# Optimization experiments

Hardware: AMD Instinct MI355X
Metric: run time of the kernel (lower is better)

Reference implementation:

```python
import jax, jax.numpy as jnp
import numpy as np

D = 384      # embedding_dim
H = 6        # num_heads
HD = D // H  # head_dim = 64
S = 256      # seq_len
B = 64       # batch
EPS = 1e-5


def setup_inputs() -> dict:
    key = jax.random.key(0)
    ks = jax.random.split(key, 16)
    scale = 0.02
    inp = {
        'x': jax.random.normal(ks[0], (B, S, D), dtype=jnp.float32),
        'wq': jax.random.normal(ks[1], (D, D), dtype=jnp.float32) * scale,
        'wk': jax.random.normal(ks[2], (D, D), dtype=jnp.float32) * scale,
        'wv': jax.random.normal(ks[3], (D, D), dtype=jnp.float32) * scale,
        'wo': jax.random.normal(ks[4], (D, D), dtype=jnp.float32) * scale,
        'bo': jnp.zeros((D,), dtype=jnp.float32),
        'w1': jax.random.normal(ks[5], (D, 4 * D), dtype=jnp.float32) * scale,
        'b1': jnp.zeros((4 * D,), dtype=jnp.float32),
        'w2': jax.random.normal(ks[6], (4 * D, D), dtype=jnp.float32) * scale,
        'b2': jnp.zeros((D,), dtype=jnp.float32),
        'g1': jnp.ones((D,), dtype=jnp.float32),
        'be1': jnp.zeros((D,), dtype=jnp.float32),
        'g2': jnp.ones((D,), dtype=jnp.float32),
        'be2': jnp.zeros((D,), dtype=jnp.float32),
    }
    return inp


def _layernorm(x, g, b):
    m = jnp.mean(x, axis=-1, keepdims=True)
    v = jnp.mean((x - m) ** 2, axis=-1, keepdims=True)
    return (x - m) * jax.lax.rsqrt(v + EPS) * g + b


def _block(x, wq, wk, wv, wo, bo, w1, b1, w2, b2, g1, be1, g2, be2):
    b, s, d = x.shape
    h = _layernorm(x, g1, be1)
    # batched per-head projections (equivalent to 6 separate small Linears concatenated)
    q = (h @ wq).reshape(b, s, H, HD).transpose(0, 2, 1, 3)  # [B,H,S,HD]
    k = (h @ wk).reshape(b, s, H, HD).transpose(0, 2, 1, 3)
    v = (h @ wv).reshape(b, s, H, HD).transpose(0, 2, 1, 3)
    scores = jnp.einsum('bhqe,bhke->bhqk', q, k) / np.float32(np.sqrt(HD))
    causal = jnp.tril(jnp.ones((s, s), dtype=bool))
    scores = jnp.where(causal, scores, -jnp.inf)
    attn = jax.nn.softmax(scores, axis=-1)  # dropout = identity in eval
    ctx = jnp.einsum('bhqk,bhke->bhqe', attn, v)  # [B,H,S,HD]
    ctx = ctx.transpose(0, 2, 1, 3).reshape(b, s, d)  # concat heads
    x = x + (ctx @ wo + bo)
    h2 = _layernorm(x, g2, be2)
    ff = jax.nn.relu(h2 @ w1 + b1) @ w2 + b2
    return x + ff


def reference(x, wq, wk, wv, wo, bo, w1, b1, w2, b2, g1, be1, g2, be2):
    return _block(x, wq, wk, wv, wo, bo, w1, b1, w2, b2, g1, be1, g2, be2)
```

## Files before the change

kernel.cpp:

```cpp
#include <hip/hip_runtime.h>
#include <hip/hip_bf16.h>

typedef __hip_bfloat16 bf16;
typedef __attribute__((ext_vector_type(8))) short short8;
typedef __attribute__((ext_vector_type(4))) float f32x4;

#define D_EMB 384
#define NHEAD 6
#define HDIM 64
#define SEQ 256
#define BATCH 64
#define M_ROWS (BATCH * SEQ)
#define DFF (4 * D_EMB)
#define DQKV (3 * D_EMB)

__device__ __forceinline__ void async_load16(const void* gptr, void* lptr) {
    __builtin_amdgcn_global_load_lds(
        (const __attribute__((address_space(1))) unsigned int*)gptr,
        (__attribute__((address_space(3))) unsigned int*)lptr, 16, 0, 0);
}

__global__ __launch_bounds__(256)
void transpose_all(const float* __restrict__ wq, const float* __restrict__ wk,
                   const float* __restrict__ wv, const float* __restrict__ wo,
                   const float* __restrict__ w1, const float* __restrict__ w2,
                   bf16* __restrict__ wqkv_t, bf16* __restrict__ wo_t,
                   bf16* __restrict__ w1_t, bf16* __restrict__ w2_t)
{
    __shared__ float t[32][33];
    const int id = blockIdx.x;
    const float* src; bf16* dst; int K, N, local, nbT;
    if      (id <  144) { src = wq; dst = wqkv_t;               K = 384;  N = 384;  local = id;        nbT = 12; }
    else if (id <  288) { src = wk; dst = wqkv_t + 147456;      K = 384;  N = 384;  local = id - 144;  nbT = 12; }
    else if (id <  432) { src = wv; dst = wqkv_t + 294912;      K = 384;  N = 384;  local = id - 288;  nbT = 12; }
    else if (id <  576) { src = wo; dst = wo_t;                 K = 384;  N = 384;  local = id - 432;  nbT = 12; }
    else if (id < 1152) { src = w1; dst = w1_t;                 K = 384;  N = 1536; local = id - 576;  nbT = 48; }
    else                { src = w2; dst = w2_t;                 K = 1536; N = 384;  local = id - 1152; nbT = 12; }
    const int nb = (local % nbT) * 32, kb = (local / nbT) * 32;
    const int tx = threadIdx.x, ty = threadIdx.y;
#pragma unroll
    for (int i = 0; i < 32; i += 8)
        t[ty + i][tx] = src[(size_t)(kb + ty + i) * N + nb + tx];
    __syncthreads();
#pragma unroll
    for (int i = 0; i < 32; i += 8)
        dst[(size_t)(nb + ty + i) * K + kb + tx] = __float2bfloat16(t[tx][ty + i]);
}

__global__ __launch_bounds__(256)
void ln_kernel(const float* __restrict__ x, const float* __restrict__ g,
               const float* __restrict__ be, bf16* __restrict__ out)
{
    const int row  = blockIdx.x * 4 + (threadIdx.x >> 6);
    const int lane = threadIdx.x & 63;
    const float* xr = x + (size_t)row * D_EMB;

    float v[6];
    float s = 0.f;
#pragma unroll
    for (int i = 0; i < 6; ++i) { v[i] = xr[lane + i * 64]; s += v[i]; }
#pragma unroll
    for (int off = 32; off; off >>= 1) s += __shfl_xor(s, off, 64);
    const float mean = s * (1.f / 384.f);

    float var = 0.f;
#pragma unroll
    for (int i = 0; i < 6; ++i) { float d = v[i] - mean; var += d * d; }
#pragma unroll
    for (int off = 32; off; off >>= 1) var += __shfl_xor(var, off, 64);
    const float rstd = rsqrtf(var * (1.f / 384.f) + 1e-5f);

    bf16* orow = out + (size_t)row * D_EMB;
#pragma unroll
    for (int i = 0; i < 6; ++i) {
        const int c = lane + i * 64;
        orow[c] = __float2bfloat16((v[i] - mean) * rstd * g[c] + be[c]);
    }
}

template<bool RELU, bool OUT_BF16, bool VT>
__global__ __launch_bounds__(256)
void mfma_gemm(const bf16* __restrict__ A, const bf16* __restrict__ Bt,
               const float* __restrict__ bias, const float* __restrict__ res,
               void* __restrict__ Cout, int M, int N, int K, bf16* __restrict__ vt)
{
    __shared__ __attribute__((aligned(16))) unsigned short smem[32768];
    unsigned short* As = smem;
    unsigned short* Bs = smem + 16384;

    const int tid  = threadIdx.x;
    const int wave = tid >> 6;
    const int lane = tid & 63;

    const int nwg = gridDim.x * gridDim.y;
    const int bl  = blockIdx.y * gridDim.x + blockIdx.x;
    const int lb  = (bl & 7) * (nwg >> 3) + (bl >> 3);
    const int m0  = (lb / gridDim.x) * 128;
    const int n0  = (lb % gridDim.x) * 128;

    const int wm = (wave >> 1) * 64;
    const int wn = (wave & 1) * 64;
    const int c16 = lane & 15;
    const int g   = lane >> 4;
    const int lr  = lane >> 3;
    const int ls  = lane & 7;

    f32x4 acc[4][4];
#pragma unroll
    for (int i = 0; i < 4; ++i)
#pragma unroll
        for (int j = 0; j < 4; ++j)
            acc[i][j] = (f32x4){0.f, 0.f, 0.f, 0.f};

    auto stage = [&](int buf, int k0) {
#pragma unroll
        for (int it = 0; it < 4; ++it) {
            const int r = (it * 4 + wave) * 8 + lr;
            const int oct = ls ^ (r & 7);
            async_load16(A + (size_t)(m0 + r) * K + k0 + oct * 8,
                         &As[buf * 8192 + (it * 4 + wave) * 512]);
            async_load16(Bt + (size_t)(n0 + r) * K + k0 + oct * 8,
                         &Bs[buf * 8192 + (it * 4 + wave) * 512]);
        }
    };

    stage(0, 0);
    const int KT = K >> 6;
    for (int kt = 0; kt < KT; ++kt) {
        const int cur = kt & 1;
        __syncthreads();
        if (kt + 1 < KT) stage(cur ^ 1, (kt + 1) * 64);
#pragma unroll
        for (int kk = 0; kk < 2; ++kk) {
            short8 af[4], bfr[4];
#pragma unroll
            for (int i = 0; i < 4; ++i) {
                const int row = wm + i * 16 + c16;
                af[i] = *(const short8*)&As[cur * 8192 + row * 64 + (((kk * 4 + g) ^ (row & 7)) << 3)];
            }
#pragma unroll
            for (int j = 0; j < 4; ++j) {
                const int row = wn + j * 16 + c16;
                bfr[j] = *(const short8*)&Bs[cur * 8192 + row * 64 + (((kk * 4 + g) ^ (row & 7)) << 3)];
            }
#pragma unroll
            for (int i = 0; i < 4; ++i)
#pragma unroll
                for (int j = 0; j < 4; ++j)
                    acc[i][j] = __builtin_amdgcn_mfma_f32_16x16x32_bf16(
                        af[i], bfr[j], acc[i][j], 0, 0, 0);
        }
    }

    const int crow = g * 4;

    if (VT && n0 >= 768) {
        __syncthreads();
        unsigned short* T = smem;
#pragma unroll
        for (int j = 0; j < 4; ++j) {
            const int col = wn + j * 16 + c16;
#pragma unroll
            for (int i = 0; i < 4; ++i)
#pragma unroll
                for (int r = 0; r < 4; ++r) {
                    const int row = wm + i * 16 + crow + r;
                    bf16 pb = __float2bfloat16(acc[i][j][r]);
                    T[col * 128 + ((((row >> 3) ^ (col & 15)) << 3) | (row & 7))] =
                        *(unsigned short*)&pb;
                }
        }
        __syncthreads();
        const int b  = m0 >> 8;
        const int s0 = m0 & 255;
#pragma unroll
        for (int it = 0; it < 8; ++it) {
            const int cc = it * 256 + tid;
            const int col = cc >> 4, o = cc & 15;
            const int gcol = n0 - 768 + col;
            const int h = gcol >> 6, d = gcol & 63;
            const int so = (o ^ (col & 15)) << 3;
            const uint4 v = *(const uint4*)&T[col * 128 + o * 8];
            *(uint4*)(vt + (((size_t)(b * NHEAD + h) * 64 + d) * 256 + s0 + so)) = v;
        }
        return;
    }

    if (OUT_BF16) {
        __syncthreads();
        unsigned short* Cs = smem;
#pragma unroll
        for (int j = 0; j < 4; ++j) {
            const int col = wn + j * 16 + c16;
            const float bv = bias ? bias[n0 + col] : 0.f;
#pragma unroll
            for (int i = 0; i < 4; ++i)
#pragma unroll
                for (int r = 0; r < 4; ++r) {
                    const int row = wm + i * 16 + crow + r;
                    float v = acc[i][j][r] + bv;
                    if (RELU) v = fmaxf(v, 0.f);
                    bf16 pb = __float2bfloat16(v);
                    Cs[row * 128 + ((((col >> 3) ^ (row & 15)) << 3) | (col & 7))] =
                        *(unsigned short*)&pb;
                }
        }
        __syncthreads();
#pragma unroll
        for (int it = 0; it < 8; ++it) {
            const int cc = it * 256 + tid;
            const int row = cc >> 4, o = cc & 15;
            const uint4 v = *(const uint4*)&Cs[row * 128 + ((o ^ (row & 15)) << 3)];
            *(uint4*)((bf16*)Cout + (size_t)(m0 + row) * N + n0 + o * 8) = v;
        }
        return;
    }

#pragma unroll
    for (int j = 0; j < 4; ++j) {
        const int colg = n0 + wn + j * 16 + c16;
        const float bv = bias ? bias[colg] : 0.f;
#pragma unroll
        for (int i = 0; i < 4; ++i) {
            const int rowg = m0 + wm + i * 16 + crow;
#pragma unroll
            for (int r = 0; r < 4; ++r) {
                float v = acc[i][j][r] + bv;
                if (res) v += res[(size_t)(rowg + r) * N + colg];
                if (RELU) v = fmaxf(v, 0.f);
                ((float*)Cout)[(size_t)(rowg + r) * N + colg] = v;
            }
        }
    }
}

__global__ __launch_bounds__(256)
void mfma_gemm64(const bf16* __restrict__ A, const bf16* __restrict__ Bt,
                 const float* __restrict__ bias, const float* __restrict__ res,
                 float* __restrict__ Cout, int M, int N, int K)
{
    __shared__ __attribute__((aligned(16))) unsigned short smem[24576];
    unsigned short* As = smem;
    unsigned short* Bs = smem + 8192;

    const int tid  = threadIdx.x;
    const int wave = tid >> 6;
    const int lane = tid & 63;

    const int nwg = gridDim.x * gridDim.y;
    const int bl  = blockIdx.y * gridDim.x + blockIdx.x;
    const int lb  = (bl & 7) * (nwg >> 3) + (bl >> 3);
    const int m0  = (lb / gridDim.x) * 64;
    const int n0  = (lb % gridDim.x) * 128;

    const int wm = (wave >> 1) * 32;
    const int wn = (wave & 1) * 64;
    const int c16 = lane & 15;
    const int g   = lane >> 4;
    const int lr  = lane >> 3;
    const int ls  = lane & 7;

    f32x4 acc[2][4];
#pragma unroll
    for (int i = 0; i < 2; ++i)
#pragma unroll
        for (int j = 0; j < 4; ++j)
            acc[i][j] = (f32x4){0.f, 0.f, 0.f, 0.f};

    auto stage = [&](int buf, int k0) {
#pragma unroll
        for (int it = 0; it < 2; ++it) {
            const int r = (it * 4 + wave) * 8 + lr;
            const int oct = ls ^ (r & 7);
            async_load16(A + (size_t)(m0 + r) * K + k0 + oct * 8,
                         &As[buf * 4096 + (it * 4 + wave) * 512]);
        }
#pragma unroll
        for (int it = 0; it < 4; ++it) {
            const int r = (it * 4 + wave) * 8 + lr;
            const int oct = ls ^ (r & 7);
            async_load16(Bt + (size_t)(n0 + r) * K + k0 + oct * 8,
                         &Bs[buf * 8192 + (it * 4 + wave) * 512]);
        }
    };

    stage(0, 0);
    const int KT = K >> 6;
    for (int kt = 0; kt < KT; ++kt) {
        const int cur = kt & 1;
        __syncthreads();
        if (kt + 1 < KT) stage(cur ^ 1, (kt + 1) * 64);
#pragma unroll
        for (int kk = 0; kk < 2; ++kk) {
            short8 af[2], bfr[4];
#pragma unroll
            for (int i = 0; i < 2; ++i) {
                const int row = wm + i * 16 + c16;
                af[i] = *(const short8*)&As[cur * 4096 + row * 64 + (((kk * 4 + g) ^ (row & 7)) << 3)];
            }
#pragma unroll
            for (int j = 0; j < 4; ++j) {
                const int row = wn + j * 16 + c16;
                bfr[j] = *(const short8*)&Bs[cur * 8192 + row * 64 + (((kk * 4 + g) ^ (row & 7)) << 3)];
            }
#pragma unroll
            for (int i = 0; i < 2; ++i)
#pragma unroll
                for (int j = 0; j < 4; ++j)
                    acc[i][j] = __builtin_amdgcn_mfma_f32_16x16x32_bf16(
                        af[i], bfr[j], acc[i][j], 0, 0, 0);
        }
    }

    const int crow = g * 4;
#pragma unroll
    for (int j = 0; j < 4; ++j) {
        const int colg = n0 + wn + j * 16 + c16;
        const float bv = bias ? bias[colg] : 0.f;
#pragma unroll
        for (int i = 0; i < 2; ++i) {
            const int rowg = m0 + wm + i * 16 + crow;
#pragma unroll
            for (int r = 0; r < 4; ++r) {
                float v = acc[i][j][r] + bv;
                if (res) v += res[(size_t)(rowg + r) * N + colg];
                Cout[(size_t)(rowg + r) * N + colg] = v;
            }
        }
    }
}

#define ATT_SCALE 0.18033688f

__global__ __launch_bounds__(64, 2)
void attn_mfma(const bf16* __restrict__ qkv, const bf16* __restrict__ vt,
               bf16* __restrict__ ctx)
{
    __shared__ __attribute__((aligned(16))) unsigned short bufKP[4096];
    __shared__ __attribute__((aligned(16))) unsigned short bufV[4096];

    const int nb   = gridDim.x;
    const int bid0 = blockIdx.x;
    const int bid  = (bid0 & 7) * (nb >> 3) + (bid0 >> 3);
    const int bh = bid >> 2, qi = bid & 3;
    const int b = bh / NHEAD, h = bh % NHEAD;
    const int lane = threadIdx.x;
    const int g = lane >> 4;
    const int c = lane & 15;
    const int lr = lane >> 3;
    const int ls = lane & 7;

    const size_t qbase  = (size_t)b * SEQ * DQKV + (size_t)h * HDIM;
    const size_t vtbase = (size_t)bh * HDIM * SEQ;

    short8 qf[4][2];
#pragma unroll
    for (int i = 0; i < 4; ++i)
#pragma unroll
        for (int kf = 0; kf < 2; ++kf)
            qf[i][kf] = *(const short8*)(qkv + qbase +
                (size_t)(qi * 64 + i * 16 + c) * DQKV + kf * 32 + g * 8);

    short8 ones;
#pragma unroll
    for (int e = 0; e < 8; ++e) ones[e] = (short)0x3F80;

    f32x4 acc_o[4][4], acc_l[4];
#pragma unroll
    for (int i = 0; i < 4; ++i) {
        acc_l[i] = (f32x4){0.f, 0.f, 0.f, 0.f};
#pragma unroll
        for (int n = 0; n < 4; ++n)
            acc_o[i][n] = (f32x4){0.f, 0.f, 0.f, 0.f};
    }

    for (int jt = 0; jt <= qi; ++jt) {
#pragma unroll
        for (int it = 0; it < 8; ++it) {
            const int row = it * 8 + lr;
            const int oct = ls ^ (row & 7);
            async_load16(qkv + qbase + (size_t)(jt * 64 + row) * DQKV + D_EMB + oct * 8,
                         bufKP + it * 512);
            async_load16(vt + vtbase + (size_t)row * SEQ + jt * 64 + oct * 8,
                         bufV + it * 512);
        }
        asm volatile("s_waitcnt vmcnt(0)" ::: "memory");

        short8 kb[2][4];
#pragma unroll
        for (int kf = 0; kf < 2; ++kf)
#pragma unroll
            for (int j = 0; j < 4; ++j) {
                const int row = j * 16 + c;
                kb[kf][j] = *(const short8*)&bufKP[row * 64 + (((kf * 4 + g) ^ (row & 7)) << 3)];
            }

        const bool diag = (jt == qi);
#pragma unroll
        for (int i = 0; i < 4; ++i) {
            f32x4 s[4];
#pragma unroll
            for (int j = 0; j < 4; ++j) s[j] = (f32x4){0.f, 0.f, 0.f, 0.f};
#pragma unroll
            for (int kf = 0; kf < 2; ++kf)
#pragma unroll
                for (int j = 0; j < 4; ++j)
                    s[j] = __builtin_amdgcn_mfma_f32_16x16x32_bf16(
                        qf[i][kf], kb[kf][j], s[j], 0, 0, 0);

#pragma unroll
            for (int r = 0; r < 4; ++r) {
                const int row = i * 16 + g * 4 + r;
#pragma unroll
                for (int j = 0; j < 4; ++j) {
                    const int col = j * 16 + c;
                    float p = exp2f(s[j][r] * ATT_SCALE);
                    if (diag && col > row) p = 0.f;
                    bf16 pb = __float2bfloat16(p);
                    bufKP[row * 64 + (((col >> 3) ^ (row & 7)) << 3) + (col & 7)] =
                        *(unsigned short*)&pb;
                }
            }
        }

#pragma unroll
        for (int kf = 0; kf < 2; ++kf) {
            short8 pa[4], vb[4];
#pragma unroll
            for (int i = 0; i < 4; ++i) {
                const int row = i * 16 + c;
                pa[i] = *(const short8*)&bufKP[row * 64 + (((kf * 4 + g) ^ (row & 7)) << 3)];
            }
#pragma unroll
            for (int n = 0; n < 4; ++n) {
                const int row = n * 16 + c;
                vb[n] = *(const short8*)&bufV[row * 64 + (((kf * 4 + g) ^ (row & 7)) << 3)];
            }
#pragma unroll
            for (int i = 0; i < 4; ++i) {
#pragma unroll
                for (int n = 0; n < 4; ++n)
                    acc_o[i][n] = __builtin_amdgcn_mfma_f32_16x16x32_bf16(
                        pa[i], vb[n], acc_o[i][n], 0, 0, 0);
                acc_l[i] = __builtin_amdgcn_mfma_f32_16x16x32_bf16(
                    pa[i], ones, acc_l[i], 0, 0, 0);
            }
        }
    }

    const size_t obase = (size_t)b * SEQ * D_EMB + (size_t)h * HDIM;
#pragma unroll
    for (int i = 0; i < 4; ++i)
#pragma unroll
        for (int r = 0; r < 4; ++r) {
            const float rl = 1.f / acc_l[i][r];
            const int row = qi * 64 + i * 16 + g * 4 + r;
#pragma unroll
            for (int n = 0; n < 4; ++n) {
                const int col = n * 16 + c;
                ctx[obase + (size_t)row * D_EMB + col] =
                    __float2bfloat16(acc_o[i][n][r] * rl);
            }
        }
}

extern "C" void kernel_launch(void* const* d_in, const int* in_sizes, int n_in,
                              void* d_out, int out_size, void* d_ws, size_t ws_size,
                              hipStream_t stream)
{
    const float* x  = (const float*)d_in[0];
    const float* wq = (const float*)d_in[1];
    const float* wk = (const float*)d_in[2];
    const float* wv = (const float*)d_in[3];
    const float* wo = (const float*)d_in[4];
    const float* bo = (const float*)d_in[5];
    const float* w1 = (const float*)d_in[6];
    const float* b1 = (const float*)d_in[7];
    const float* w2 = (const float*)d_in[8];
    const float* b2 = (const float*)d_in[9];
    const float* g1  = (const float*)d_in[10];
    const float* be1 = (const float*)d_in[11];
    const float* g2  = (const float*)d_in[12];
    const float* be2 = (const float*)d_in[13];
    float* out = (float*)d_out;
    (void)in_sizes; (void)n_in; (void)out_size; (void)ws_size;

    char* w = (char*)d_ws;
    bf16* wqkv_t = (bf16*)(w);
    bf16* wo_t   = (bf16*)(w + (size_t)(1024 * 1024));
    bf16* w1_t   = (bf16*)(w + (size_t)(1536 * 1024));
    bf16* w2_t   = (bf16*)(w + (size_t)(2816 * 1024));
    char* slotA  = w + 4 * 1024 * 1024;
    char* slotB  = slotA + (size_t)M_ROWS * D_EMB * sizeof(bf16);

    bf16* h1  = (bf16*)slotA;
    bf16* ctx = (bf16*)slotA;
    bf16* h2  = (bf16*)slotA;
    bf16* qkv = (bf16*)slotB;
    bf16* vt  = (bf16*)slotB + (size_t)M_ROWS * DQKV;
    bf16* ff1 = (bf16*)slotB;

    const dim3 blk(256);

    transpose_all<<<dim3(1728), dim3(32, 8), 0, stream>>>(
        wq, wk, wv, wo, w1, w2, wqkv_t, wo_t, w1_t, w2_t);

    ln_kernel<<<dim3(M_ROWS / 4), blk, 0, stream>>>(x, g1, be1, h1);

    mfma_gemm<false, true, true><<<dim3(DQKV / 128, M_ROWS / 128), blk, 0, stream>>>(
        h1, wqkv_t, nullptr, nullptr, qkv, M_ROWS, DQKV, D_EMB, vt);

    attn_mfma<<<dim3(BATCH * NHEAD * 4), dim3(64), 0, stream>>>(qkv, vt, ctx);

    mfma_gemm64<<<dim3(D_EMB / 128, M_ROWS / 64), blk, 0, stream>>>(
        ctx, wo_t, bo, x, out, M_ROWS, D_EMB, D_EMB);

    ln_kernel<<<dim3(M_ROWS / 4), blk, 0, stream>>>(out, g2, be2, h2);

    mfma_gemm<true, true, false><<<dim3(DFF / 128, M_ROWS / 128), blk, 0, stream>>>(
        h2, w1_t, b1, nullptr, ff1, M_ROWS, DFF, D_EMB, nullptr);

    mfma_gemm64<<<dim3(D_EMB / 128, M_ROWS / 64), blk, 0, stream>>>(
        ff1, w2_t, b2, out, out, M_ROWS, D_EMB, DFF);
}
```

Measured before the change: 234.7 us.

## Double-buffer K/V tiles in attention and fuse weight transpose with first LayerNorm

The attention kernel now keeps two K and two V shared-memory buffers and prefetches the next key tile while computing on the current one, waiting only on the older loads (vmcnt(16)) so global-memory latency overlaps with MFMA work. The weight transpose/convert kernel and the first LayerNorm are merged into one launch to save a kernel launch and let both run concurrently. Shared memory per attention block doubles to 32KB, which can reduce occupancy. There is also a possible hazard: P is written into the current K buffer with no barrier, although the kernel is single-wave.

Measured after the change: 259.9 us. +10.8%, slower.

```diff
diff --git a/kernel.cpp b/kernel.cpp
--- a/kernel.cpp
+++ b/kernel.cpp
@@ -21,30 +21,63 @@
 }
 
 __global__ __launch_bounds__(256)
-void transpose_all(const float* __restrict__ wq, const float* __restrict__ wk,
-                   const float* __restrict__ wv, const float* __restrict__ wo,
-                   const float* __restrict__ w1, const float* __restrict__ w2,
-                   bf16* __restrict__ wqkv_t, bf16* __restrict__ wo_t,
-                   bf16* __restrict__ w1_t, bf16* __restrict__ w2_t)
+void prep_fused(const float* __restrict__ wq, const float* __restrict__ wk,
+                const float* __restrict__ wv, const float* __restrict__ wo,
+                const float* __restrict__ w1, const float* __restrict__ w2,
+                bf16* __restrict__ wqkv_t, bf16* __restrict__ wo_t,
+                bf16* __restrict__ w1_t, bf16* __restrict__ w2_t,
+                const float* __restrict__ x, const float* __restrict__ g1,
+                const float* __restrict__ be1, bf16* __restrict__ h1)
 {
     __shared__ float t[32][33];
     const int id = blockIdx.x;
-    const float* src; bf16* dst; int K, N, local, nbT;
-    if      (id <  144) { src = wq; dst = wqkv_t;               K = 384;  N = 384;  local = id;        nbT = 12; }
-    else if (id <  288) { src = wk; dst = wqkv_t + 147456;      K = 384;  N = 384;  local = id - 144;  nbT = 12; }
-    else if (id <  432) { src = wv; dst = wqkv_t + 294912;      K = 384;  N = 384;  local = id - 288;  nbT = 12; }
-    else if (id <  576) { src = wo; dst = wo_t;                 K = 384;  N = 384;  local = id - 432;  nbT = 12; }
-    else if (id < 1152) { src = w1; dst = w1_t;                 K = 384;  N = 1536; local = id - 576;  nbT = 48; }
-    else                { src = w2; dst = w2_t;                 K = 1536; N = 384;  local = id - 1152; nbT = 12; }
-    const int nb = (local % nbT) * 32, kb = (local / nbT) * 32;
-    const int tx = threadIdx.x, ty = threadIdx.y;
-#pragma unroll
-    for (int i = 0; i < 32; i += 8)
-        t[ty + i][tx] = src[(size_t)(kb + ty + i) * N + nb + tx];
-    __syncthreads();
-#pragma unroll
-    for (int i = 0; i < 32; i += 8)
-        dst[(size_t)(nb + ty + i) * K + kb + tx] = __float2bfloat16(t[tx][ty + i]);
+    const int tid = threadIdx.x;
+
+    if (id < 1728) {
+        const float* src; bf16* dst; int K, N, local, nbT;
+        if      (id <  144) { src = wq; dst = wqkv_t;               K = 384;  N = 384;  local = id;        nbT = 12; }
+        else if (id <  288) { src = wk; dst = wqkv_t + 147456;      K = 384;  N = 384;  local = id - 144;  nbT = 12; }
+        else if (id <  432) { src = wv; dst = wqkv_t + 294912;      K = 384;  N = 384;  local = id - 288;  nbT = 12; }
+        else if (id <  576) { src = wo; dst = wo_t;                 K = 384;  N = 384;  local = id - 432;  nbT = 12; }
+        else if (id < 1152) { src = w1; dst = w1_t;                 K = 384;  N = 1536; local = id - 576;  nbT = 48; }
+        else                { src = w2; dst = w2_t;                 K = 1536; N = 384;  local = id - 1152; nbT = 12; }
+        const int nb = (local % nbT) * 32, kb = (local / nbT) * 32;
+        const int tx = tid & 31, ty = tid >> 5;
+#pragma unroll
+        for (int i = 0; i < 32; i += 8)
+            t[ty + i][tx] = src[(size_t)(kb + ty + i) * N + nb + tx];
+        __syncthreads();
+#pragma unroll
+        for (int i = 0; i < 32; i += 8)
+            dst[(size_t)(nb + ty + i) * K + kb + tx] = __float2bfloat16(t[tx][ty + i]);
+        return;
+    }
+
+    const int row  = (id - 1728) * 4 + (tid >> 6);
+    const int lane = tid & 63;
+    const float* xr = x + (size_t)row * D_EMB;
+
+    float v[6];
+    float s = 0.f;
+#pragma unroll
+    for (int i = 0; i < 6; ++i) { v[i] = xr[lane + i * 64]; s += v[i]; }
+#pragma unroll
+    for (int off = 32; off; off >>= 1) s += __shfl_xor(s, off, 64);
+    const float mean = s * (1.f / 384.f);
+
+    float var = 0.f;
+#pragma unroll
+    for (int i = 0; i < 6; ++i) { float d = v[i] - mean; var += d * d; }
+#pragma unroll
+    for (int off = 32; off; off >>= 1) var += __shfl_xor(var, off, 64);
+    const float rstd = rsqrtf(var * (1.f / 384.f) + 1e-5f);
+
+    bf16* orow = h1 + (size_t)row * D_EMB;
+#pragma unroll
+    for (int i = 0; i < 6; ++i) {
+        const int c = lane + i * 64;
+        orow[c] = __float2bfloat16((v[i] - mean) * rstd * g1[c] + be1[c]);
+    }
 }
 
 __global__ __launch_bounds__(256)
@@ -336,8 +369,8 @@
 void attn_mfma(const bf16* __restrict__ qkv, const bf16* __restrict__ vt,
                bf16* __restrict__ ctx)
 {
-    __shared__ __attribute__((aligned(16))) unsigned short bufKP[4096];
-    __shared__ __attribute__((aligned(16))) unsigned short bufV[4096];
+    __shared__ __attribute__((aligned(16))) unsigned short bufK[2][4096];
+    __shared__ __attribute__((aligned(16))) unsigned short bufV[2][4096];
 
     const int nb   = gridDim.x;
     const int bid0 = blockIdx.x;
@@ -353,38 +386,49 @@
     const size_t qbase  = (size_t)b * SEQ * DQKV + (size_t)h * HDIM;
     const size_t vtbase = (size_t)bh * HDIM * SEQ;
 
-    short8 qf[4][2];
-#pragma unroll
-    for (int i = 0; i < 4; ++i)
-#pragma unroll
-        for (int kf = 0; kf < 2; ++kf)
-            qf[i][kf] = *(const short8*)(qkv + qbase +
-                (size_t)(qi * 64 + i * 16 + c) * DQKV + kf * 32 + g * 8);
-
-    short8 ones;
-#pragma unroll
-    for (int e = 0; e < 8; ++e) ones[e] = (short)0x3F80;
-
-    f32x4 acc_o[4][4], acc_l[4];
-#pragma unroll
-    for (int i = 0; i < 4; ++i) {
-        acc_l[i] = (f32x4){0.f, 0.f, 0.f, 0.f};
-#pragma unroll
-        for (int n = 0; n < 4; ++n)
-            acc_o[i][n] = (f32x4){0.f, 0.f, 0.f, 0.f};
-    }
-
-    for (int jt = 0; jt <= qi; ++jt) {
+    auto load_tile = [&](int jt, int bsel) {
 #pragma unroll
         for (int it = 0; it < 8; ++it) {
             const int row = it * 8 + lr;
             const int oct = ls ^ (row & 7);
             async_load16(qkv + qbase + (size_t)(jt * 64 + row) * DQKV + D_EMB + oct * 8,
-                         bufKP + it * 512);
+                         &bufK[bsel][it * 512]);
             async_load16(vt + vtbase + (size_t)row * SEQ + jt * 64 + oct * 8,
-                         bufV + it * 512);
-        }
-        asm volatile("s_waitcnt vmcnt(0)" ::: "memory");
+                         &bufV[bsel][it * 512]);
+        }
+    };
+
+    load_tile(0, 0);
+
+    short8 qf[4][2];
+#pragma unroll
+    for (int i = 0; i < 4; ++i)
+#pragma unroll
+        for (int kf = 0; kf < 2; ++kf)
+            qf[i][kf] = *(const short8*)(qkv + qbase +
+                (size_t)(qi * 64 + i * 16 + c) * DQKV + kf * 32 + g * 8);
+
+    short8 ones;
+#pragma unroll
+    for (int e = 0; e < 8; ++e) ones[e] = (short)0x3F80;
+
+    f32x4 acc_o[4][4], acc_l[4];
+#pragma unroll
+    for (int i = 0; i < 4; ++i) {
+        acc_l[i] = (f32x4){0.f, 0.f, 0.f, 0.f};
+#pragma unroll
+        for (int n = 0; n < 4; ++n)
+            acc_o[i][n] = (f32x4){0.f, 0.f, 0.f, 0.f};
+    }
+
+    for (int jt = 0; jt <= qi; ++jt) {
+        const int cur = jt & 1;
+        if (jt < qi) {
+            load_tile(jt + 1, cur ^ 1);
+            asm volatile("s_waitcnt vmcnt(16)" ::: "memory");
+        } else {
+            asm volatile("s_waitcnt vmcnt(0)" ::: "memory");
+        }
 
         short8 kb[2][4];
 #pragma unroll
@@ -392,7 +436,7 @@
 #pragma unroll
             for (int j = 0; j < 4; ++j) {
                 const int row = j * 16 + c;
-                kb[kf][j] = *(const short8*)&bufKP[row * 64 + (((kf * 4 + g) ^ (row & 7)) << 3)];
+                kb[kf][j] = *(const short8*)&bufK[cur][row * 64 + (((kf * 4 + g) ^ (row & 7)) << 3)];
             }
 
         const bool diag = (jt == qi);
@@ -417,7 +461,7 @@
                     float p = exp2f(s[j][r] * ATT_SCALE);
                     if (diag && col > row) p = 0.f;
                     bf16 pb = __float2bfloat16(p);
-                    bufKP[row * 64 + (((col >> 3) ^ (row & 7)) << 3) + (col & 7)] =
+                    bufK[cur][row * 64 + (((col >> 3) ^ (row & 7)) << 3) + (col & 7)] =
                         *(unsigned short*)&pb;
                 }
             }
@@ -429,12 +473,12 @@
 #pragma unroll
             for (int i = 0; i < 4; ++i) {
                 const int row = i * 16 + c;
-                pa[i] = *(const short8*)&bufKP[row * 64 + (((kf * 4 + g) ^ (row & 7)) << 3)];
+                pa[i] = *(const short8*)&bufK[cur][row * 64 + (((kf * 4 + g) ^ (row & 7)) << 3)];
             }
 #pragma unroll
             for (int n = 0; n < 4; ++n) {
                 const int row = n * 16 + c;
-                vb[n] = *(const short8*)&bufV[row * 64 + (((kf * 4 + g) ^ (row & 7)) << 3)];
+                vb[n] = *(const short8*)&bufV[cur][row * 64 + (((kf * 4 + g) ^ (row & 7)) << 3)];
             }
 #pragma unroll
             for (int i = 0; i < 4; ++i) {
@@ -502,10 +546,8 @@
 
     const dim3 blk(256);
 
-    transpose_all<<<dim3(1728), dim3(32, 8), 0, stream>>>(
-        wq, wk, wv, wo, w1, w2, wqkv_t, wo_t, w1_t, w2_t);
-
-    ln_kernel<<<dim3(M_ROWS / 4), blk, 0, stream>>>(x, g1, be1, h1);
+    prep_fused<<<dim3(1728 + M_ROWS / 4), blk, 0, stream>>>(
+        wq, wk, wv, wo, w1, w2, wqkv_t, wo_t, w1_t, w2_t, x, g1, be1, h1);
 
     mfma_gemm<false, true, true><<<dim3(DQKV / 128, M_ROWS / 128), blk, 0, stream>>>(
         h1, wqkv_t, nullptr, nullptr, qkv, M_ROWS, DQKV, D_EMB, vt);
```
